# Optimization experiments

Measured on AMD Instinct MI355X. Metric: run time of the kernel, lower is better.

## Reference

```python
import jax, jax.numpy as jnp
import numpy as np
from jax import lax

FEAT_STRIDE = 16
SCALES = (8.0, 16.0, 32.0)
RATIOS = (0.5, 1.0, 2.0)
PRE_NMS_TOPN = 6000
POST_NMS_TOPN = 300
NMS_THRESH = 0.5
MIN_SIZE = 16.0


def _generate_anchors(base_size=16.0):
    # Faithful Caffe generate_anchors: ratio enumeration outer, scale inner.
    w = h = base_size
    x_ctr = y_ctr = (base_size - 1.0) / 2.0
    size = w * h
    anchors = []
    for r in RATIOS:
        ws = np.round(np.sqrt(size / r))
        hs = np.round(ws * r)
        for s in SCALES:
            W = ws * s
            H = hs * s
            anchors.append([x_ctr - (W - 1) / 2.0, y_ctr - (H - 1) / 2.0,
                            x_ctr + (W - 1) / 2.0, y_ctr + (H - 1) / 2.0])
    return np.asarray(anchors, dtype=np.float32)  # (A=9, 4)


def _nms_keep(boxes, thresh):
    # boxes sorted by descending score; returns bool keep mask. JIT-friendly.
    n = boxes.shape[0]
    x1, y1, x2, y2 = boxes[:, 0], boxes[:, 1], boxes[:, 2], boxes[:, 3]
    areas = (x2 - x1 + 1.0) * (y2 - y1 + 1.0)
    xx1 = jnp.maximum(x1[:, None], x1[None, :])
    yy1 = jnp.maximum(y1[:, None], y1[None, :])
    xx2 = jnp.minimum(x2[:, None], x2[None, :])
    yy2 = jnp.minimum(y2[:, None], y2[None, :])
    inter = jnp.maximum(xx2 - xx1 + 1.0, 0.0) * jnp.maximum(yy2 - yy1 + 1.0, 0.0)
    iou = inter / (areas[:, None] + areas[None, :] - inter)  # (n, n)
    idxs = jnp.arange(n)

    def body(i, keep):
        suppress = (iou[i] > thresh) & keep[i] & (idxs > i)
        return keep & ~suppress

    return lax.fori_loop(0, n, body, jnp.ones((n,), dtype=bool))


def _proposal(scores, bbox_deltas):
    # scores: (1, H, W, 2A) rpn class probs; bbox_deltas: (1, H, W, 4A)
    _, H, W, A4 = bbox_deltas.shape
    A = A4 // 4
    im_h = jnp.float32(H * FEAT_STRIDE)
    im_w = jnp.float32(W * FEAT_STRIDE)

    anchors = jnp.asarray(_generate_anchors())  # (A, 4)
    shift_x = jnp.arange(W, dtype=jnp.float32) * FEAT_STRIDE
    shift_y = jnp.arange(H, dtype=jnp.float32) * FEAT_STRIDE
    sx, sy = jnp.meshgrid(shift_x, shift_y)  # (H, W) row-major like Caffe
    shifts = jnp.stack([sx.ravel(), sy.ravel(), sx.ravel(), sy.ravel()], axis=1)  # (K, 4)
    all_anchors = (anchors[None, :, :] + shifts[:, None, :]).reshape(-1, 4)  # (K*A, 4)

    fg_scores = scores[0, :, :, A:].reshape(-1)        # (K*A,) fg probs
    deltas = bbox_deltas[0].reshape(-1, 4)             # (K*A, 4)

    # bbox_transform_inv (Caffe convention with +1 widths)
    aw = all_anchors[:, 2] - all_anchors[:, 0] + 1.0
    ah = all_anchors[:, 3] - all_anchors[:, 1] + 1.0
    acx = all_anchors[:, 0] + 0.5 * aw
    acy = all_anchors[:, 1] + 0.5 * ah
    dx, dy, dw, dh = deltas[:, 0], deltas[:, 1], deltas[:, 2], deltas[:, 3]
    pcx = dx * aw + acx
    pcy = dy * ah + acy
    pw = jnp.exp(dw) * aw
    ph = jnp.exp(dh) * ah
    x1 = jnp.clip(pcx - 0.5 * pw, 0.0, im_w - 1.0)
    y1 = jnp.clip(pcy - 0.5 * ph, 0.0, im_h - 1.0)
    x2 = jnp.clip(pcx + 0.5 * pw, 0.0, im_w - 1.0)
    y2 = jnp.clip(pcy + 0.5 * ph, 0.0, im_h - 1.0)
    proposals = jnp.stack([x1, y1, x2, y2], axis=1)  # (K*A, 4)

    # min_size filter (im scale = 1): mask score to -inf instead of removing
    ws = x2 - x1 + 1.0
    hs = y2 - y1 + 1.0
    valid = (ws >= MIN_SIZE) & (hs >= MIN_SIZE)
    masked_scores = jnp.where(valid, fg_scores, -jnp.inf)

    top_scores, order = lax.top_k(masked_scores, PRE_NMS_TOPN)
    top_boxes = proposals[order]  # (pre_nms, 4), score-descending

    keep = _nms_keep(lax.stop_gradient(top_boxes), NMS_THRESH)
    keep = keep & jnp.isfinite(top_scores)

    n = PRE_NMS_TOPN
    ranked = jnp.where(keep, jnp.arange(n), n)
    picked = jnp.sort(ranked)[:POST_NMS_TOPN]  # first kept in score order
    ok = picked < n
    picked_c = jnp.minimum(picked, n - 1)
    out_boxes = top_boxes[picked_c] * ok[:, None].astype(top_boxes.dtype)

    # normalized proposals in [0, 1]
    scale = jnp.array([im_w, im_h, im_w, im_h], dtype=top_boxes.dtype)
    return out_boxes / scale  # (post_nms_topN, 4)


def setup_inputs() -> dict:
    key = jax.random.key(0)
    k1, k2 = jax.random.split(key)
    scores = jax.random.uniform(k1, (1, 64, 64, 18), dtype=jnp.float32)
    bbox_deltas = jax.random.normal(k2, (1, 64, 64, 36), dtype=jnp.float32)
    return {"scores": scores, "bbox_deltas": bbox_deltas}


def reference(scores, bbox_deltas):
    return _proposal(scores, bbox_deltas)
```

## Files before the change

kernel.cpp:

```cpp
#include <hip/hip_runtime.h>
#include <math.h>


#define NPROP   36864
#define TOPN    6000
#define POSTN   300
#define NWORDS  94
#define NROUND  47
#define MAXSEL  8192
#define NB      16384
#define SPLIT   8
#define NEGINF_PAT 0x007FFFFFu

typedef unsigned long long u64;

__constant__ float ANCH[9][4] = {
    {-84.f,  -40.f,  99.f,  55.f},
    {-176.f, -88.f,  191.f, 103.f},
    {-360.f, -184.f, 375.f, 199.f},
    {-56.f,  -56.f,  71.f,  71.f},
    {-120.f, -120.f, 135.f, 135.f},
    {-248.f, -248.f, 263.f, 263.f},
    {-36.f,  -80.f,  51.f,  95.f},
    {-80.f,  -168.f, 95.f,  183.f},
    {-168.f, -344.f, 183.f, 359.f},
};

__device__ __forceinline__ float4 decode_box(const float* __restrict__ deltas, int i,
                                             bool* valid_out) {
    int a   = i % 9;
    int pos = i / 9;
    int wx = pos & 63, hy = pos >> 6;
    float sx = (float)(wx * 16), sy = (float)(hy * 16);
    float ax1 = ANCH[a][0] + sx, ay1 = ANCH[a][1] + sy;
    float ax2 = ANCH[a][2] + sx, ay2 = ANCH[a][3] + sy;
    float aw  = ax2 - ax1 + 1.0f;
    float ah  = ay2 - ay1 + 1.0f;
    float acx = ax1 + 0.5f * aw;
    float acy = ay1 + 0.5f * ah;
    float4 d4 = ((const float4*)deltas)[i];
    float pcx = __fadd_rn(__fmul_rn(d4.x, aw), acx);
    float pcy = __fadd_rn(__fmul_rn(d4.y, ah), acy);
    float pw  = __fmul_rn(expf(d4.z), aw);
    float ph  = __fmul_rn(expf(d4.w), ah);
    float hx  = __fmul_rn(0.5f, pw);
    float hv  = __fmul_rn(0.5f, ph);
    float x1 = fminf(fmaxf(__fsub_rn(pcx, hx), 0.0f), 1023.0f);
    float y1 = fminf(fmaxf(__fsub_rn(pcy, hv), 0.0f), 1023.0f);
    float x2 = fminf(fmaxf(__fadd_rn(pcx, hx), 0.0f), 1023.0f);
    float y2 = fminf(fmaxf(__fadd_rn(pcy, hv), 0.0f), 1023.0f);
    float bw = __fadd_rn(__fsub_rn(x2, x1), 1.0f);
    float bh = __fadd_rn(__fsub_rn(y2, y1), 1.0f);
    *valid_out = (bw >= 16.0f) && (bh >= 16.0f);
    return make_float4(x1, y1, x2, y2);
}

__device__ __forceinline__ float box_area(float4 b) {
    return __fmul_rn(__fadd_rn(__fsub_rn(b.z, b.x), 1.0f),
                     __fadd_rn(__fsub_rn(b.w, b.y), 1.0f));
}

__global__ __launch_bounds__(256) void decode_kernel(
        const float* __restrict__ scores,
        const float* __restrict__ deltas,
        unsigned* __restrict__ uhigh) {
    int i = blockIdx.x * 256 + threadIdx.x;
    bool valid;
    (void)decode_box(deltas, i, &valid);
    int a = i % 9, pos = i / 9;
    float fg = scores[(size_t)pos * 18 + 9 + a];
    float sc = valid ? fg : -__builtin_huge_valf();
    unsigned u = __float_as_uint(sc);
    u = (u & 0x80000000u) ? ~u : (u | 0x80000000u);
    uhigh[i] = u;
}

__global__ __launch_bounds__(1024) void select_compact(
        const unsigned* __restrict__ uhigh,
        u64* __restrict__ sel,
        unsigned* __restrict__ nsel) {
    __shared__ unsigned hist[NB];
    __shared__ unsigned strip[1024];
    __shared__ unsigned group[64];
    __shared__ unsigned thr_sh, cnt_sh;
    int t = threadIdx.x, lane = t & 63;
    #pragma unroll
    for (int r = 0; r < NB / 1024; ++r) hist[t + r * 1024] = 0;
    if (t == 0) cnt_sh = 0;
    __syncthreads();

    unsigned v[36];
    #pragma unroll
    for (int r = 0; r < 36; ++r) v[r] = uhigh[t + r * 1024];
    #pragma unroll
    for (int r = 0; r < 36; ++r) atomicAdd(&hist[v[r] >> 18], 1u);
    __syncthreads();

    unsigned s = 0;
    #pragma unroll
    for (int k = 0; k < 16; ++k) s += hist[t * 16 + k];
    strip[t] = s;
    __syncthreads();
    if (t < 64) {
        unsigned g = 0;
        #pragma unroll
        for (int k = 0; k < 16; ++k) g += strip[t * 16 + k];
        group[t] = g;
    }
    __syncthreads();
    if (t == 0) {
        unsigned acc = 0; int g = 63;
        while (g > 0 && acc + group[g] < TOPN) { acc += group[g]; --g; }
        int si = g * 16 + 15;
        while (si > g * 16 && acc + strip[si] < TOPN) { acc += strip[si]; --si; }
        int b = si * 16 + 15;
        while (b > si * 16 && acc + hist[b] < TOPN) { acc += hist[b]; --b; }
        thr_sh = (unsigned)b;
    }
    __syncthreads();
    unsigned thr = thr_sh << 18;
    #pragma unroll
    for (int r = 0; r < 36; ++r) {
        bool pred = (v[r] >= thr);
        u64 b = __ballot(pred);
        int nb = __popcll(b);
        unsigned base = 0;
        if (lane == 0 && nb) base = atomicAdd(&cnt_sh, (unsigned)nb);
        base = __shfl(base, 0, 64);
        if (pred) {
            unsigned p = base + (unsigned)__popcll(b & ((1ULL << lane) - 1ULL));
            if (p < MAXSEL)
                sel[p] = ((u64)v[r] << 32) |
                         (u64)(0xFFFFFFFFu - (unsigned)(t + r * 1024));
        }
    }
    __syncthreads();
    if (t == 0) *nsel = (cnt_sh > MAXSEL) ? MAXSEL : cnt_sh;
}

__global__ __launch_bounds__(256) void rank_partial(
        const u64* __restrict__ sel,
        const unsigned* __restrict__ nsel,
        int* __restrict__ rank8) {
    __shared__ u64 tile[1024];
    int t = threadIdx.x;
    int j = blockIdx.x * 256 + t;
    int n = (int)*nsel;
    int T = (n + SPLIT - 1) / SPLIT;
    int lo = blockIdx.y * T;
    int hi = min(lo + T, n);
    u64 myk = (j < n) ? sel[j] : 0ULL;
    int rk = 0;
    for (int base = lo; base < hi; base += 1024) {
        int m = min(1024, hi - base);
        for (int q = t; q < m; q += 256) tile[q] = sel[base + q];
        __syncthreads();
        #pragma unroll 4
        for (int q = 0; q < m; ++q) rk += (tile[q] > myk) ? 1 : 0;
        __syncthreads();
    }
    rank8[blockIdx.y * MAXSEL + j] = rk;
}

__global__ __launch_bounds__(256) void scatter_top(
        const u64* __restrict__ sel,
        const unsigned* __restrict__ nsel,
        const int* __restrict__ rank8,
        const float* __restrict__ deltas,
        float4* __restrict__ topb,
        float* __restrict__ areas,
        unsigned* __restrict__ topu) {
    int j = blockIdx.x * 256 + threadIdx.x;
    int n = (int)*nsel;
    if (j >= n) return;
    int r = 0;
    #pragma unroll
    for (int s = 0; s < SPLIT; ++s) r += rank8[s * MAXSEL + j];
    if (r >= TOPN) return;
    u64 k = sel[j];
    unsigned idx = 0xFFFFFFFFu - (unsigned)(k & 0xFFFFFFFFull);
    bool valid;
    float4 b = decode_box(deltas, (int)idx, &valid);
    topb[r] = b;
    areas[r] = box_area(b);
    topu[r] = (unsigned)(k >> 32);
}

__global__ void nms_mask(const float4* __restrict__ boxes,
                         const float* __restrict__ areas,
                         u64* __restrict__ mask) {
    int rb = blockIdx.x, cb = blockIdx.y;
    if (cb < rb) return;
    __shared__ float4 cbx[64];
    __shared__ float  car[64];
    int tid = threadIdx.x;
    int j0 = cb * 64;
    if (j0 + tid < TOPN) { cbx[tid] = boxes[j0 + tid]; car[tid] = areas[j0 + tid]; }
    __syncthreads();
    int i = rb * 64 + tid;
    if (i >= TOPN) return;
    float4 bi = boxes[i];
    float  ai = areas[i];
    u64 bits = 0ULL;
    int jmax = min(64, TOPN - j0);
    for (int jj = 0; jj < jmax; ++jj) {
        int j = j0 + jj;
        if (j <= i) continue;
        float4 bj = cbx[jj];
        float xx1 = fmaxf(bi.x, bj.x);
        float yy1 = fmaxf(bi.y, bj.y);
        float xx2 = fminf(bi.z, bj.z);
        float yy2 = fminf(bi.w, bj.w);
        float w = fmaxf(__fadd_rn(__fsub_rn(xx2, xx1), 1.0f), 0.0f);
        float h = fmaxf(__fadd_rn(__fsub_rn(yy2, yy1), 1.0f), 0.0f);
        float inter = __fmul_rn(w, h);
        float denom = __fsub_rn(__fadd_rn(ai, car[jj]), inter);
        float iou = inter / denom;
        if (iou > 0.5f) bits |= (1ULL << jj);
    }
    mask[(size_t)i * NWORDS + cb] = bits;
}

__global__ __launch_bounds__(1024) void nms_scan(
        const u64* __restrict__ mask,
        const unsigned* __restrict__ topu,
        const float4* __restrict__ topb,
        float* __restrict__ out) {
    __shared__ unsigned rem32[NWORDS * 2];
    __shared__ u64 diag[2][128][4];
    __shared__ u64 Fsh[2][2];
    __shared__ short kept_rows[2][128];
    __shared__ short kept_list[POSTN];
    __shared__ int nk_sh[2];
    __shared__ int cnt_sh, stop_sh;

    int t = threadIdx.x, wave = t >> 6, lane = t & 63;
    if (t >= 640 && t < 640 + NWORDS * 2) rem32[t - 640] = 0;
    if (t >= 128 && t < 640) {
        int idx = t - 128;
        diag[0][idx >> 2][idx & 3] = mask[(size_t)(idx >> 2) * NWORDS + (idx & 3)];
    }
    if (wave == 0) {
        u64 f = __ballot(topu[lane] != NEGINF_PAT);
        if (lane == 0) { Fsh[0][0] = f; cnt_sh = 0; stop_sh = 0; nk_sh[0] = 0; nk_sh[1] = 0; }
    } else if (wave == 1) {
        u64 f = __ballot(topu[64 + lane] != NEGINF_PAT);
        if (lane == 0) Fsh[0][1] = f;
    }
    __syncthreads();

    u64 urg0 = 0, urg1 = 0;

    for (int r = 0; r < NROUND; ++r) {
        int p = r & 1;
        int i0 = r * 128;
        if (wave == 0) {
            u64 r0w0 = diag[p][lane][0];
            u64 r0w1 = diag[p][lane][1];
            u64 r1w1 = diag[p][64 + lane][1];
            u64 R0 = ((u64)rem32[4 * r]     | ((u64)rem32[4 * r + 1] << 32)) | urg0;
            u64 R1 = ((u64)rem32[4 * r + 2] | ((u64)rem32[4 * r + 3] << 32)) | urg1;
            int nb = min(128, TOPN - i0);
            u64 v1 = (nb >= 128) ? ~0ULL : ((1ULL << (nb - 64)) - 1ULL);
            u64 a0 = ~R0;
            u64 a1 = ~R1 & v1;
            u64 k0 = 0ULL, k1 = 0ULL;
            while (a0) {
                int ii = __builtin_ctzll(a0);
                u64 bit = 1ULL << ii;
                k0 |= bit;
                u64 s0 = __shfl(r0w0, ii, 64);
                u64 s1 = __shfl(r0w1, ii, 64);
                a0 &= ~(s0 | bit);
                a1 &= ~s1;
            }
            while (a1) {
                int ii = __builtin_ctzll(a1);
                u64 bit = 1ULL << ii;
                k1 |= bit;
                u64 s1 = __shfl(r1w1, ii, 64);
                a1 &= ~(s1 | bit);
            }
            u64 F0 = Fsh[p][0], F1 = Fsh[p][1];
            u64 kf0 = k0 & F0, kf1 = k1 & F1;
            int nk0 = __popcll(k0);
            int c0  = __popcll(kf0);
            int base = cnt_sh;
            u64 ltm = (1ULL << lane) - 1ULL;
            if ((k0 >> lane) & 1)
                kept_rows[p][__popcll(k0 & ltm)] = (short)(i0 + lane);
            if ((k1 >> lane) & 1)
                kept_rows[p][nk0 + __popcll(k1 & ltm)] = (short)(i0 + 64 + lane);
            if ((kf0 >> lane) & 1) {
                int pos = base + __popcll(kf0 & ltm);
                if (pos < POSTN) kept_list[pos] = (short)(i0 + lane);
            }
            if ((kf1 >> lane) & 1) {
                int pos = base + c0 + __popcll(kf1 & ltm);
                if (pos < POSTN) kept_list[pos] = (short)(i0 + 64 + lane);
            }
            u64 a0u = 0ULL, a1u = 0ULL;
            if ((k0 >> lane) & 1) { a0u = diag[p][lane][2];       a1u = diag[p][lane][3]; }
            if ((k1 >> lane) & 1) { a0u |= diag[p][64 + lane][2]; a1u |= diag[p][64 + lane][3]; }
            #pragma unroll
            for (int off = 1; off < 64; off <<= 1) {
                a0u |= __shfl_xor(a0u, off, 64);
                a1u |= __shfl_xor(a1u, off, 64);
            }
            urg0 = a0u; urg1 = a1u;
            if (lane == 0) {
                nk_sh[p] = nk0 + __popcll(k1);
                int cc = base + c0 + __popcll(kf1);
                if (cc > POSTN) cc = POSTN;
                cnt_sh = cc;
                stop_sh = (cc >= POSTN) || (r == NROUND - 1);
            }
        } else if (wave == 15) {
            if (r + 1 < NROUND) {
                int i1 = i0 + 128;
                #pragma unroll
                for (int q = lane; q < 512; q += 64) {
                    int row = i1 + (q >> 2), k = q & 3;
                    int wd = 2 * (r + 1) + k;
                    diag[p ^ 1][q >> 2][k] = (row < TOPN && wd < NWORDS)
                        ? mask[(size_t)row * NWORDS + wd] : 0ULL;
                }
                u64 fa = __ballot((i1 + lane < TOPN) && (topu[i1 + lane] != NEGINF_PAT));
                u64 fb = __ballot((i1 + 64 + lane < TOPN) && (topu[i1 + 64 + lane] != NEGINF_PAT));
                if (lane == 0) { Fsh[p ^ 1][0] = fa; Fsh[p ^ 1][1] = fb; }
            }
        } else {
            int nkp = nk_sh[p ^ 1];
            int left = NWORDS - (2 * r + 2);
            if (r > 0 && nkp > 0 && left > 0) {
                int tot = nkp * left;
                for (int q = t - 64; q < tot; q += 896) {
                    int k  = q / left;
                    int wd = 2 * r + 2 + (q - k * left);
                    int row = kept_rows[p ^ 1][k];
                    u64 v = mask[(size_t)row * NWORDS + wd];
                    if (v) {
                        unsigned lo = (unsigned)v, hi = (unsigned)(v >> 32);
                        if (lo) atomicOr(&rem32[2 * wd],     lo);
                        if (hi) atomicOr(&rem32[2 * wd + 1], hi);
                    }
                }
            }
        }
        __syncthreads();
        if (stop_sh) break;
    }

    if (t < POSTN) {
        float4 v = make_float4(0.f, 0.f, 0.f, 0.f);
        if (t < cnt_sh) {
            float4 b = topb[kept_list[t]];
            const float s = 0.0009765625f;
            v = make_float4(b.x * s, b.y * s, b.z * s, b.w * s);
        }
        ((float4*)out)[t] = v;
    }
}

extern "C" void kernel_launch(void* const* d_in, const int* in_sizes, int n_in,
                              void* d_out, int out_size, void* d_ws, size_t ws_size,
                              hipStream_t stream) {
    const float* scores = (const float*)d_in[0];
    const float* deltas = (const float*)d_in[1];
    float* out = (float*)d_out;

    char* w = (char*)d_ws;
    unsigned* uhigh = (unsigned*)(w);
    u64*      sel   = (u64*)(w + 147456);
    unsigned* nsel  = (unsigned*)(w + 212992);
    int*      rank8 = (int*)(w + 213008);
    float4*   topb  = (float4*)(w + 475152);
    float*    areas = (float*)(w + 571152);
    unsigned* topu  = (unsigned*)(w + 595152);
    u64*      mask  = (u64*)(w + 619152);

    decode_kernel<<<NPROP / 256, 256, 0, stream>>>(scores, deltas, uhigh);
    select_compact<<<1, 1024, 0, stream>>>(uhigh, sel, nsel);
    rank_partial<<<dim3(MAXSEL / 256, SPLIT), 256, 0, stream>>>(sel, nsel, rank8);
    scatter_top<<<MAXSEL / 256, 256, 0, stream>>>(sel, nsel, rank8, deltas, topb, areas, topu);
    nms_mask<<<dim3(NWORDS, NWORDS), 64, 0, stream>>>(topb, areas, mask);
    nms_scan<<<1, 1024, 0, stream>>>(mask, topu, topb, out);
}
```

Measured before the change: 145.2 us.

## Build score histogram in decode kernel and select threshold with wave scans

Moves histogram construction out of the single-block select kernel. The 144 decode blocks now each build a shared-memory histogram and merge it into a global histogram with atomics. Threshold search changes from a serial thread-0 walk to wave-level suffix scans with ballots. The aim is to cut the serial single-block phase, at the cost of an extra memset, a 16K-entry shared clear and flush in every decode block, and global atomics.

```diff
diff --git a/kernel.cpp b/kernel.cpp
--- a/kernel.cpp
+++ b/kernel.cpp
@@ -63,8 +63,15 @@
 __global__ __launch_bounds__(256) void decode_kernel(
         const float* __restrict__ scores,
         const float* __restrict__ deltas,
-        unsigned* __restrict__ uhigh) {
-    int i = blockIdx.x * 256 + threadIdx.x;
+        unsigned* __restrict__ uhigh,
+        unsigned* __restrict__ ghist) {
+    __shared__ unsigned h[NB];
+    int t = threadIdx.x;
+    #pragma unroll
+    for (int r = 0; r < NB / 256; ++r) h[t + r * 256] = 0;
+    __syncthreads();
+
+    int i = blockIdx.x * 256 + t;
     bool valid;
     (void)decode_box(deltas, i, &valid);
     int a = i % 9, pos = i / 9;
@@ -73,55 +80,79 @@
     unsigned u = __float_as_uint(sc);
     u = (u & 0x80000000u) ? ~u : (u | 0x80000000u);
     uhigh[i] = u;
+    atomicAdd(&h[u >> 18], 1u);
+    __syncthreads();
+
+    #pragma unroll
+    for (int r = 0; r < NB / 256; ++r) {
+        unsigned v = h[t + r * 256];
+        if (v) atomicAdd(&ghist[t + r * 256], v);
+    }
 }
 
 __global__ __launch_bounds__(1024) void select_compact(
+        const unsigned* __restrict__ ghist,
         const unsigned* __restrict__ uhigh,
         u64* __restrict__ sel,
         unsigned* __restrict__ nsel) {
-    __shared__ unsigned hist[NB];
     __shared__ unsigned strip[1024];
-    __shared__ unsigned group[64];
     __shared__ unsigned thr_sh, cnt_sh;
-    int t = threadIdx.x, lane = t & 63;
-    #pragma unroll
-    for (int r = 0; r < NB / 1024; ++r) hist[t + r * 1024] = 0;
+    int t = threadIdx.x, lane = t & 63, wave = t >> 6;
+
+    const uint4* g4 = (const uint4*)ghist;
+    uint4 qa = g4[t * 4 + 0], qb = g4[t * 4 + 1], qc = g4[t * 4 + 2], qd = g4[t * 4 + 3];
+    unsigned s = qa.x + qa.y + qa.z + qa.w + qb.x + qb.y + qb.z + qb.w
+               + qc.x + qc.y + qc.z + qc.w + qd.x + qd.y + qd.z + qd.w;
+    strip[t] = s;
     if (t == 0) cnt_sh = 0;
     __syncthreads();
 
-    unsigned v[36];
-    #pragma unroll
-    for (int r = 0; r < 36; ++r) v[r] = uhigh[t + r * 1024];
-    #pragma unroll
-    for (int r = 0; r < 36; ++r) atomicAdd(&hist[v[r] >> 18], 1u);
-    __syncthreads();
-
-    unsigned s = 0;
-    #pragma unroll
-    for (int k = 0; k < 16; ++k) s += hist[t * 16 + k];
-    strip[t] = s;
-    __syncthreads();
-    if (t < 64) {
+    if (wave == 0) {
         unsigned g = 0;
         #pragma unroll
-        for (int k = 0; k < 16; ++k) g += strip[t * 16 + k];
-        group[t] = g;
-    }
-    __syncthreads();
-    if (t == 0) {
-        unsigned acc = 0; int g = 63;
-        while (g > 0 && acc + group[g] < TOPN) { acc += group[g]; --g; }
-        int si = g * 16 + 15;
-        while (si > g * 16 && acc + strip[si] < TOPN) { acc += strip[si]; --si; }
-        int b = si * 16 + 15;
-        while (b > si * 16 && acc + hist[b] < TOPN) { acc += hist[b]; --b; }
-        thr_sh = (unsigned)b;
-    }
-    __syncthreads();
-    unsigned thr = thr_sh << 18;
-    #pragma unroll
+        for (int k = 0; k < 16; ++k) g += strip[lane * 16 + k];
+        unsigned suf = g;
+        #pragma unroll
+        for (int off = 1; off < 64; off <<= 1) {
+            unsigned x = __shfl_down(suf, off, 64);
+            if (lane + off < 64) suf += x;
+        }
+        u64 bal = __ballot(suf >= TOPN);
+        int gsel = 63 - __builtin_clzll(bal);
+        unsigned rest = __shfl(suf, (gsel < 63) ? gsel + 1 : 63, 64);
+        if (gsel == 63) rest = 0;
+
+        unsigned sv = (lane < 16) ? strip[gsel * 16 + lane] : 0;
+        unsigned suf2 = sv;
+        #pragma unroll
+        for (int off = 1; off < 16; off <<= 1) {
+            unsigned x = __shfl_down(suf2, off, 64);
+            if (lane + off < 16) suf2 += x;
+        }
+        u64 bal2 = __ballot((lane < 16) && (rest + suf2 >= TOPN));
+        int ssel = 63 - __builtin_clzll(bal2);
+        unsigned rest2 = __shfl(suf2, (ssel < 15) ? ssel + 1 : 15, 64);
+        if (ssel == 15) rest2 = 0;
+        rest2 += rest;
+        int S = gsel * 16 + ssel;
+
+        unsigned bv = (lane < 16) ? ghist[S * 16 + lane] : 0;
+        unsigned suf3 = bv;
+        #pragma unroll
+        for (int off = 1; off < 16; off <<= 1) {
+            unsigned x = __shfl_down(suf3, off, 64);
+            if (lane + off < 16) suf3 += x;
+        }
+        u64 bal3 = __ballot((lane < 16) && (rest2 + suf3 >= TOPN));
+        int bsel = 63 - __builtin_clzll(bal3);
+        if (lane == 0) thr_sh = ((unsigned)(S * 16 + bsel)) << 18;
+    }
+    __syncthreads();
+    unsigned thr = thr_sh;
+
     for (int r = 0; r < 36; ++r) {
-        bool pred = (v[r] >= thr);
+        unsigned u = uhigh[t + r * 1024];
+        bool pred = (u >= thr);
         u64 b = __ballot(pred);
         int nb = __popcll(b);
         unsigned base = 0;
@@ -130,7 +161,7 @@
         if (pred) {
             unsigned p = base + (unsigned)__popcll(b & ((1ULL << lane) - 1ULL));
             if (p < MAXSEL)
-                sel[p] = ((u64)v[r] << 32) |
+                sel[p] = ((u64)u << 32) |
                          (u64)(0xFFFFFFFFu - (unsigned)(t + r * 1024));
         }
     }
@@ -377,10 +408,12 @@
     float4*   topb  = (float4*)(w + 475152);
     float*    areas = (float*)(w + 571152);
     unsigned* topu  = (unsigned*)(w + 595152);
-    u64*      mask  = (u64*)(w + 619152);
-
-    decode_kernel<<<NPROP / 256, 256, 0, stream>>>(scores, deltas, uhigh);
-    select_compact<<<1, 1024, 0, stream>>>(uhigh, sel, nsel);
+    unsigned* ghist = (unsigned*)(w + 619152);
+    u64*      mask  = (u64*)(w + 684688);
+
+    hipMemsetAsync(ghist, 0, NB * sizeof(unsigned), stream);
+    decode_kernel<<<NPROP / 256, 256, 0, stream>>>(scores, deltas, uhigh, ghist);
+    select_compact<<<1, 1024, 0, stream>>>(ghist, uhigh, sel, nsel);
     rank_partial<<<dim3(MAXSEL / 256, SPLIT), 256, 0, stream>>>(sel, nsel, rank8);
     scatter_top<<<MAXSEL / 256, 256, 0, stream>>>(sel, nsel, rank8, deltas, topb, areas, topu);
     nms_mask<<<dim3(NWORDS, NWORDS), 64, 0, stream>>>(topb, areas, mask);
```

Measured after the change: 153.0 us. +5.4%, slower.
